# Kernel optimization log

Measured on AMD Instinct MI355X. Metric: run time of the kernel, lower is better.

## Reference

```python
import jax, jax.numpy as jnp
import numpy as np

N = 50000   # nodes
E = 600000  # edges / hyperedge incidences
D = 128     # node_in_dim
H = 128     # hidden_dim
TAU = 0.5
ALPHA = 0.5
LAM = 0.5

_PARAM_SHAPES = [('Wq0', (1, H)), ('bq0', (H,)), ('W0', (D, H)), ('b0', (H,)),
                 ('Whq0', (1, H)), ('bhq0', (H,)), ('Wh0', (D, H)), ('bh0', (H,)),
                 ('Wf0', (H, H)), ('bf0', (H,)), ('Wfh0', (H, H)), ('bfh0', (H,)),
                 ('aq0', (H,)), ('a0', (H,)), ('ahq0', (H,)), ('ah0', (H,)),
                 ('aq_', (H,)), ('a_', (H,)), ('ahq_', (H,)), ('ah_', (H,)),
                 ('Wlq', (1, H)), ('blq', (H,)), ('Wlf', (D, H)), ('blf', (H,)),
                 ('Wm1', (H, H)), ('bm1', (H,)), ('Wm2', (H, H)), ('bm2', (H,))]


def setup_inputs() -> dict:
    key = jax.random.key(0)
    ks = jax.random.split(key, 8 + len(_PARAM_SHAPES))
    inp = {}
    inp['feats'] = jax.random.normal(ks[0], (N, D), dtype=jnp.float32)
    inp['edge_index'] = jax.random.randint(ks[1], (2, E), 0, N).astype(jnp.int32)
    inp['edge_index_aug'] = jax.random.randint(ks[2], (2, E), 0, N).astype(jnp.int32)
    inp['pos'] = jax.random.randint(ks[3], (100,), 1, N).astype(jnp.int32)
    inp['q'] = 0
    for i, (nm, sh) in enumerate(_PARAM_SHAPES):
        inp[nm] = jax.random.normal(ks[4 + i], sh, dtype=jnp.float32) * 0.05
    return inp


def _forward(feats, Wq0, bq0, W0, b0, Whq0, bhq0, Wh0, bh0, Wf0, bf0, Wfh0, bfh0,
             aq0, a0, ahq0, ah0, aq_, a_, ahq_, ah_, Wlq, blq, Wlf, blf,
             Wm1, bm1, Wm2, bm2, edge_index, edge_index_aug, q, pos):
    # ---- GCNConv (PyG default: add self-loops + symmetric normalization) ----
    sl = jnp.arange(N, dtype=edge_index.dtype)
    src = jnp.concatenate([edge_index[0], sl])
    dst = jnp.concatenate([edge_index[1], sl])
    deg = jax.ops.segment_sum(jnp.ones(src.shape[0], jnp.float32), dst, num_segments=N)
    dinv = jax.lax.rsqrt(deg)  # deg >= 1 thanks to self-loops
    enorm = dinv[src] * dinv[dst]

    def gcn(x, W, b):
        xw = x @ W
        return jax.ops.segment_sum(xw[src] * enorm[:, None], dst, num_segments=N) + b

    # ---- HypergraphConv (PyG, no attention): X' = D^-1 H B^-1 H^T X W ----
    node = edge_index_aug[0]
    he = edge_index_aug[1]
    Be = jax.ops.segment_sum(jnp.ones((E,), jnp.float32), he, num_segments=N)
    Dn = jax.ops.segment_sum(jnp.ones((E,), jnp.float32), node, num_segments=N)
    Binv = jnp.where(Be > 0, 1.0 / Be, 0.0)
    Dninv = jnp.where(Dn > 0, 1.0 / Dn, 0.0)

    def hg(x, W, b):
        xw = x @ W
        me = jax.ops.segment_sum(xw[node], he, num_segments=N) * Binv[:, None]
        return jax.ops.segment_sum(me[he], node, num_segments=N) * Dninv[:, None] + b

    # ---- attention-weighted fusion of two views (softmax over 2 logits) ----
    def fuse(a, b, wa, wb):
        att = jax.nn.softmax(jnp.stack([a @ wa, b @ wb], axis=1), axis=1)  # [N,2]
        return att[:, 0:1] * a + att[:, 1:2] * b

    querys = jnp.zeros((N, 1), jnp.float32).at[q].set(1.0)
    hq = jax.nn.relu(gcn(querys, Wq0, bq0))
    h = jax.nn.relu(gcn(feats, W0, b0))
    hf = fuse(hq, h, aq0, a0)
    h_augq = jax.nn.relu(hg(querys, Whq0, bhq0))
    h_aug = jax.nn.relu(hg(feats, Wh0, bh0))
    h_augf = fuse(h_augq, h_aug, ahq0, ah0)
    querys2 = querys @ Wlq + blq
    feats2 = feats @ Wlf + blf
    hf_ = fuse(querys2, feats2, aq_, a_)
    hf = jax.nn.relu(hf + gcn(hf_, Wf0, bf0))
    hfh_ = fuse(querys2, feats2, ahq_, ah_)
    h_augf = jax.nn.relu(h_augf + hg(hfh_, Wfh0, bfh0))

    def mlp(x):
        return jax.nn.relu(x @ Wm1 + bm1) @ Wm2 + bm2

    z = mlp(hf)
    z_aug = mlp(h_augf)

    # ---- Contra loss ----
    def expcos(v, M):
        num = M @ v
        den = jnp.maximum(jnp.linalg.norm(M, axis=1) * jnp.linalg.norm(v), 1e-8)
        return jnp.exp(num / den / TAU)

    sim1 = expcos(z[q], z)
    sim_aug1 = expcos(z_aug[q], z_aug)
    sim2 = expcos(z[q], z_aug)
    sim_aug2 = expcos(z_aug[q], z)
    mask = jnp.zeros((N,), bool).at[pos].set(True).at[q].set(False)
    nmask = jnp.sum(mask).astype(jnp.float32)

    def nlm(s):  # mean over positives of -log(s_i / sum(s))
        r = jnp.log(jnp.sum(s)) - jnp.log(s)
        return jnp.sum(jnp.where(mask, r, 0.0)) / nmask

    loss_intra = 0.5 * (nlm(sim1) + nlm(sim_aug1))
    loss_inter = 0.5 * (nlm(sim2) + nlm(sim_aug2))
    z_unsup = jnp.log(jnp.sum(sim2)) - jnp.log(sim2[q])
    z_aug_unsup = jnp.log(jnp.sum(sim_aug2)) - jnp.log(sim_aug2[q])
    loss_unsup = 0.5 * z_unsup + 0.5 * z_aug_unsup
    return loss_intra + ALPHA * loss_inter + LAM * loss_unsup


def reference(feats, Wq0, bq0, W0, b0, Whq0, bhq0, Wh0, bh0, Wf0, bf0, Wfh0, bfh0,
              aq0, a0, ahq0, ah0, aq_, a_, ahq_, ah_, Wlq, blq, Wlf, blf,
              Wm1, bm1, Wm2, bm2, edge_index, edge_index_aug, q, pos):
    return _forward(feats, Wq0, bq0, W0, b0, Whq0, bhq0, Wh0, bh0, Wf0, bf0, Wfh0, bfh0,
                    aq0, a0, ahq0, ah0, aq_, a_, ahq_, ah_, Wlq, blq, Wlf, blf,
                    Wm1, bm1, Wm2, bm2, edge_index, edge_index_aug, q, pos)
```

## Files before the change

### kernel.cpp

```cpp
#include <hip/hip_runtime.h>

#define NN 50000
#define EE 600000
#define HH 128
#define TAU_INV 2.0f
#define PSZ 6250
#define CAP 48

#define BINB 512
#define BUFC 240
#define QCAP 80000
#define QPAD 16
#define WSUB 32
#define SUBN 196

typedef __attribute__((ext_vector_type(8))) short short8;
typedef __attribute__((ext_vector_type(4))) float f32x4;
typedef __attribute__((ext_vector_type(2))) float floatx2;

__device__ __forceinline__ float wsum64(float v) {
#pragma unroll
  for (int m = 32; m >= 1; m >>= 1) v += __shfl_xor(v, m, 64);
  return v;
}
__device__ __forceinline__ unsigned short f2bf(float f) {
  unsigned u = __builtin_bit_cast(unsigned, f);
  u = u + 0x7FFFu + ((u >> 16) & 1u);
  return (unsigned short)(u >> 16);
}
__device__ __forceinline__ float bf2f(unsigned short h) {
  unsigned u = ((unsigned)h) << 16;
  return __builtin_bit_cast(float, u);
}
__device__ __forceinline__ unsigned char fp8_enc1(float v) {
  int p = __builtin_amdgcn_cvt_pk_fp8_f32(v, v, 0, false);
  return (unsigned char)(p & 0xFF);
}
__device__ __forceinline__ void fp8x8_dec(uint2 v, float* f) {
  floatx2 a = __builtin_amdgcn_cvt_pk_f32_fp8(v.x, false);
  floatx2 b = __builtin_amdgcn_cvt_pk_f32_fp8(v.x, true);
  floatx2 c = __builtin_amdgcn_cvt_pk_f32_fp8(v.y, false);
  floatx2 d = __builtin_amdgcn_cvt_pk_f32_fp8(v.y, true);
  f[0] = a.x; f[1] = a.y; f[2] = b.x; f[3] = b.y;
  f[4] = c.x; f[5] = c.y; f[6] = d.x; f[7] = d.y;
}
__device__ __forceinline__ uint2 fp8x8_enc(const float* f) {
  int w0 = __builtin_amdgcn_cvt_pk_fp8_f32(f[0], f[1], 0, false);
  w0 = __builtin_amdgcn_cvt_pk_fp8_f32(f[2], f[3], w0, true);
  int w1 = __builtin_amdgcn_cvt_pk_fp8_f32(f[4], f[5], 0, false);
  w1 = __builtin_amdgcn_cvt_pk_fp8_f32(f[6], f[7], w1, true);
  return make_uint2((unsigned)w0, (unsigned)w1);
}

#define LDSW 136

__global__ __launch_bounds__(256) void bin_k(const int* __restrict__ ei,
                                             const int* __restrict__ ea,
                                             int* __restrict__ qcnt,
                                             unsigned int* __restrict__ qdata,
                                             const int* __restrict__ pos,
                                             const int* __restrict__ qp,
                                             int* __restrict__ maskI) {
  __shared__ int cnt[24], base[24], pfx[25];
  __shared__ unsigned int buf[24 * BUFC];
  const int tid = threadIdx.x;
  if (tid < 24) cnt[tid] = 0;
  if (blockIdx.x == 0 && tid < 100) maskI[pos[tid]] = 1;
  __syncthreads();
  if (blockIdx.x == 0 && tid == 0) maskI[*qp] = 0;
  for (int e = blockIdx.x * 256 + tid; e < EE; e += BINB * 256) {
    int pay0 = __builtin_nontemporal_load(ei + e);
    int k0 = __builtin_nontemporal_load(ei + EE + e);
    int pay1 = __builtin_nontemporal_load(ea + e);
    int k1 = __builtin_nontemporal_load(ea + EE + e);
    int k2 = pay1, pay2 = k1;
    int g0 = k0 / PSZ;
    int g1 = 8 + k1 / PSZ;
    int g2 = 16 + k2 / PSZ;
    int o0 = atomicAdd(&cnt[g0], 1);
    int o1 = atomicAdd(&cnt[g1], 1);
    int o2 = atomicAdd(&cnt[g2], 1);
    if (o0 < BUFC) buf[g0 * BUFC + o0] = ((unsigned)k0 << 16) | (unsigned)pay0;
    if (o1 < BUFC) buf[g1 * BUFC + o1] = ((unsigned)k1 << 16) | (unsigned)pay1;
    if (o2 < BUFC) buf[g2 * BUFC + o2] = ((unsigned)k2 << 16) | (unsigned)pay2;
  }
  __syncthreads();
  if (tid < 24) {
    int c = min(cnt[tid], BUFC);
    cnt[tid] = c;
    base[tid] = atomicAdd(&qcnt[tid * QPAD], c);
  }
  __syncthreads();
  if (tid == 0) {
    int s = 0;
#pragma unroll
    for (int g = 0; g < 24; ++g) { pfx[g] = s; s += cnt[g]; }
    pfx[24] = s;
  }
  __syncthreads();
  const int total = pfx[24];
  for (int j = tid; j < total; j += 256) {
    int lo2 = 0, hi2 = 24;
    while (lo2 + 1 < hi2) {
      int mid = (lo2 + hi2) >> 1;
      if (j >= pfx[mid]) lo2 = mid; else hi2 = mid;
    }
    int g = lo2;
    int i = j - pfx[g];
    int dq = base[g] + i;
    if (dq < QCAP) qdata[(size_t)g * QCAP + dq] = buf[g * BUFC + i];
  }
}

__global__ __launch_bounds__(256) void fillp_k(const int* __restrict__ qcnt,
                                               const unsigned int* __restrict__ qdata,
                                               int* __restrict__ cursor,
                                               unsigned short* __restrict__ slotsA,
                                               unsigned short* __restrict__ slotsB,
                                               unsigned short* __restrict__ slotsC,
                                               float* __restrict__ cntq,
                                               const int* __restrict__ qp,
                                               float* __restrict__ dinv,
                                               float* __restrict__ Binv,
                                               float* __restrict__ Dninv) {
  __shared__ int cur[SUBN];
  const int w = blockIdx.x;
  const int p = w & 7;
  const int r = (w >> 3) % 3;
  const int s = w / 24;
  const int lo = p * PSZ + s * SUBN;
  const int hi = min(lo + SUBN, (p + 1) * PSZ);
  const int tid = threadIdx.x;
  if (tid < SUBN) cur[tid] = 0;
  __syncthreads();
  const int g = r * 8 + p;
  const int qlen = min(qcnt[g * QPAD], QCAP);
  const unsigned int* qd = qdata + (size_t)g * QCAP;
  unsigned short* slots = (r == 0) ? slotsA : (r == 1) ? slotsB : slotsC;
  const int q = *qp;
  auto proc = [&](unsigned int rec) {
    int key = (int)(rec >> 16);
    if (key >= lo && key < hi) {
      int pay = (int)(rec & 0xFFFFu);
      int idx = atomicAdd(&cur[key - lo], 1);
      if (idx < CAP) slots[key * CAP + idx] = (unsigned short)pay;
      if (r == 1 && pay == q) atomicAdd(&cntq[key], 1.0f);
    }
  };
  const int nv4 = qlen >> 2;
  const uint4* qd4 = (const uint4*)qd;
  int j = tid;
  for (; j + 256 < nv4; j += 512) {
    uint4 r0 = qd4[j];
    uint4 r1 = qd4[j + 256];
    proc(r0.x); proc(r0.y); proc(r0.z); proc(r0.w);
    proc(r1.x); proc(r1.y); proc(r1.z); proc(r1.w);
  }
  if (j < nv4) {
    uint4 r0 = qd4[j];
    proc(r0.x); proc(r0.y); proc(r0.z); proc(r0.w);
  }
  int i = (nv4 << 2) + tid;
  if (i < qlen) proc(qd[i]);
  __syncthreads();
  for (int k = lo + tid; k < hi; k += 256) {
    int c = cur[k - lo];
    cursor[r * NN + k] = c;
    if (r == 0) dinv[k] = rsqrtf((float)(c + 1));
    else if (r == 1) Binv[k] = (c > 0) ? 1.0f / (float)c : 0.0f;
    else Dninv[k] = (c > 0) ? 1.0f / (float)c : 0.0f;
  }
}

__device__ __forceinline__ void shq_body(const int* __restrict__ ei, const int* __restrict__ ea,
                                         const int* __restrict__ qp,
                                         const float* __restrict__ dinv,
                                         const float* __restrict__ Binv,
                                         const float* __restrict__ cntq,
                                         float* __restrict__ s_hq, float* __restrict__ s_hgq,
                                         int bid) {
  int e = bid * 256 + threadIdx.x;
  if (e >= EE) return;
  int q = *qp;
  int src = __builtin_nontemporal_load(ei + e);
  if (src == q) {
    int dst = __builtin_nontemporal_load(ei + EE + e);
    atomicAdd(&s_hq[dst], dinv[q] * dinv[dst]);
  }
  int he = __builtin_nontemporal_load(ea + EE + e);
  float cq = cntq[he];
  if (cq != 0.0f) {
    int node = __builtin_nontemporal_load(ea + e);
    atomicAdd(&s_hgq[node], Binv[he] * cq);
  }
  if (e == 0) atomicAdd(&s_hq[q], dinv[q] * dinv[q]);
}

__device__ __forceinline__ void fuse2_body(const unsigned short* __restrict__ f2,
                                           const int* __restrict__ qp,
                                           const float* __restrict__ Wlq,
                                           const float* __restrict__ blq,
                                           const float* __restrict__ aq1,
                                           const float* __restrict__ a1,
                                           const float* __restrict__ aq2,
                                           const float* __restrict__ a2,
                                           unsigned short* __restrict__ out1,
                                           unsigned short* __restrict__ out2, int bid) {
  int row = bid * 4 + (threadIdx.x >> 6);
  if (row >= NN) return;
  int lane = threadIdx.x & 63;
  int c0 = lane, c1 = lane + 64;
  int q = *qp;
  float q20 = blq[c0] + ((row == q) ? Wlq[c0] : 0.f);
  float q21 = blq[c1] + ((row == q) ? Wlq[c1] : 0.f);
  float f0 = bf2f(f2[(size_t)row * 128 + c0]);
  float f1 = bf2f(f2[(size_t)row * 128 + c1]);
  float dq1 = wsum64(q20 * aq1[c0] + q21 * aq1[c1]);
  float df1 = wsum64(f0 * a1[c0] + f1 * a1[c1]);
  float dq2 = wsum64(q20 * aq2[c0] + q21 * aq2[c1]);
  float df2 = wsum64(f0 * a2[c0] + f1 * a2[c1]);
  {
    float mx = fmaxf(dq1, df1);
    float e0 = expf(dq1 - mx), e1 = expf(df1 - mx);
    float w0 = e0 / (e0 + e1), w1 = 1.f - w0;
    out1[(size_t)row * 128 + c0] = f2bf(w0 * q20 + w1 * f0);
    out1[(size_t)row * 128 + c1] = f2bf(w0 * q21 + w1 * f1);
  }
  {
    float mx = fmaxf(dq2, df2);
    float e0 = expf(dq2 - mx), e1 = expf(df2 - mx);
    float w0 = e0 / (e0 + e1), w1 = 1.f - w0;
    out2[(size_t)row * 128 + c0] = f2bf(w0 * q20 + w1 * f0);
    out2[(size_t)row * 128 + c1] = f2bf(w0 * q21 + w1 * f1);
  }
}

__global__ __launch_bounds__(256) void f2_k(const int* __restrict__ ei,
                                            const int* __restrict__ ea,
                                            const int* __restrict__ qp,
                                            const float* __restrict__ dinv,
                                            const float* __restrict__ Binv,
                                            const float* __restrict__ cntq,
                                            float* __restrict__ s_hq,
                                            float* __restrict__ s_hgq,
                                            const unsigned short* __restrict__ B6,
                                            const float* __restrict__ Wlq,
                                            const float* __restrict__ blq,
                                            const float* __restrict__ aq_,
                                            const float* __restrict__ a_,
                                            const float* __restrict__ ahq_,
                                            const float* __restrict__ ah_,
                                            unsigned short* __restrict__ B3,
                                            unsigned short* __restrict__ B4, int eb) {
  int b = blockIdx.x;
  if (b < eb)
    shq_body(ei, ea, qp, dinv, Binv, cntq, s_hq, s_hgq, b);
  else
    fuse2_body(B6, qp, Wlq, blq, aq_, a_, ahq_, ah_, B3, B4, b - eb);
}

__global__ void pack_k(const float* __restrict__ W0, const float* __restrict__ Wh0,
                       const float* __restrict__ Wlf, const float* __restrict__ Wf0,
                       const float* __restrict__ Wfh0, const float* __restrict__ Wm1,
                       const float* __restrict__ Wm2, unsigned short* __restrict__ out) {
  int tid = blockIdx.x * 256 + threadIdx.x;
  if (tid >= 7 * 2048) return;
  int mat = tid >> 11, r = tid & 2047;
  int s = r >> 9, c = (r >> 6) & 7, lane = r & 63;
  const float* W = (mat == 0) ? W0 : (mat == 1) ? Wh0 : (mat == 2) ? Wlf
                 : (mat == 3) ? Wf0 : (mat == 4) ? Wfh0 : (mat == 5) ? Wm1 : Wm2;
  int k0 = 32 * s + (lane >> 4) * 8;
  int n = 16 * c + (lane & 15);
  unsigned short* o = out + (size_t)tid * 8;
#pragma unroll
  for (int j = 0; j < 8; ++j) o[j] = f2bf(W[(k0 + j) * 128 + n]);
}

template <bool BIAS, bool RELU, int OM>
__device__ __forceinline__ void gemm_core(unsigned short* As, const short8* Wp,
                                          const float* bias, void* outv, int r0, int nrows,
                                          int tid) {
  const int wave = tid >> 6, lane = tid & 63;
  const int quad = lane >> 4, l15 = lane & 15;
  f32x4 acc[8];
#pragma unroll
  for (int c = 0; c < 8; ++c) acc[c] = (f32x4){0.f, 0.f, 0.f, 0.f};
#pragma unroll
  for (int s = 0; s < 4; ++s) {
    short8 a = *(const short8*)&As[(wave * 16 + l15) * LDSW + s * 32 + quad * 8];
#pragma unroll
    for (int c = 0; c < 8; ++c) {
      short8 b = Wp[(s * 8 + c) * 64 + lane];
      acc[c] = __builtin_amdgcn_mfma_f32_16x16x32_bf16(a, b, acc[c], 0, 0, 0);
    }
  }
  __syncthreads();
  const int rwl = wave * 16 + quad * 4;
  if (OM == 2) {
    unsigned char* l8 = (unsigned char*)As;
#pragma unroll
    for (int c = 0; c < 8; ++c) {
      int col = c * 16 + l15;
      float bv = BIAS ? bias[col] : 0.f;
#pragma unroll
      for (int r = 0; r < 4; ++r) {
        float v = acc[c][r] + bv;
        if (RELU) v = fmaxf(v, 0.f);
        l8[(rwl + r) * 128 + col] = fp8_enc1(v);
      }
    }
    __syncthreads();
#pragma unroll
    for (int t = 0; t < 2; ++t) {
      int idx = (t * 256 + tid) * 16;
      int row = idx >> 7, off = idx & 127;
      int grow = r0 + row;
      if (grow < nrows)
        *(uint4*)&((unsigned char*)outv)[(size_t)grow * 256 + off] = *(uint4*)&l8[idx];
    }
  } else {
    unsigned short* l16 = As;
#pragma unroll
    for (int c = 0; c < 8; ++c) {
      int col = c * 16 + l15;
      float bv = BIAS ? bias[col] : 0.f;
#pragma unroll
      for (int r = 0; r < 4; ++r) {
        float v = acc[c][r] + bv;
        if (RELU) v = fmaxf(v, 0.f);
        l16[(rwl + r) * 128 + col] = f2bf(v);
      }
    }
    __syncthreads();
#pragma unroll
    for (int t = 0; t < 4; ++t) {
      int idx = (t * 256 + tid) * 16;
      int row = idx >> 8, off = idx & 255;
      int grow = r0 + row;
      if (grow < nrows)
        *(uint4*)&((unsigned char*)outv)[(size_t)grow * 256 + off] =
            *(uint4*)&((unsigned char*)l16)[idx];
    }
  }
}

__device__ __forceinline__ void stage_bf16(const unsigned short* A, unsigned short* As,
                                           int r0, int nrows, int tid) {
#pragma unroll
  for (int t = 0; t < 4; ++t) {
    int v = t * 256 + tid;
    int row = v >> 4, cc = v & 15;
    int gr = r0 + row;
    uint4 val = make_uint4(0, 0, 0, 0);
    if (gr < nrows) val = ((const uint4*)A)[(size_t)gr * 16 + cc];
    *(uint4*)&As[row * LDSW + cc * 8] = val;
  }
}

template <bool BIAS, bool RELU, int OM>
__global__ __launch_bounds__(256) void gemm2_mfma(const unsigned short* __restrict__ A0,
                                                  const unsigned short* __restrict__ A1,
                                                  const short8* __restrict__ Wp0,
                                                  const short8* __restrict__ Wp1,
                                                  const float* __restrict__ b0,
                                                  const float* __restrict__ b1,
                                                  void* __restrict__ o0, void* __restrict__ o1,
                                                  int nrows, int nblk) {
  __shared__ unsigned short As[64 * LDSW];
  int b = blockIdx.x;
  const unsigned short* A = A0;
  const short8* Wp = Wp0;
  const float* bias = b0;
  void* o = o0;
  if (b >= nblk) {
    b -= nblk; A = A1; Wp = Wp1; bias = b1; o = o1;
  }
  const int r0 = b * 64;
  stage_bf16(A, As, r0, nrows, threadIdx.x);
  __syncthreads();
  gemm_core<BIAS, RELU, OM>(As, Wp, bias, o, r0, nrows, threadIdx.x);
}

__global__ __launch_bounds__(256) void gemm3_mfma(const float* __restrict__ A,
                                                  const short8* __restrict__ Wp,
                                                  const float* __restrict__ bias2,
                                                  unsigned char* __restrict__ p1,
                                                  unsigned char* __restrict__ p2,
                                                  unsigned short* __restrict__ out2,
                                                  int nrows) {
  __shared__ unsigned short As[64 * LDSW];
  const int tid = threadIdx.x;
  const int bh = blockIdx.x & 1;
  const int r0 = (blockIdx.x >> 1) * 64;
#pragma unroll
  for (int t = 0; t < 8; ++t) {
    int v = t * 256 + tid;
    int row = v >> 5, c4 = v & 31;
    int gr = r0 + row;
    f32x4 val = (f32x4){0.f, 0.f, 0.f, 0.f};
    if (gr < nrows) val = ((const f32x4*)A)[(size_t)gr * 32 + c4];
    ushort4 o;
    o.x = f2bf(val.x); o.y = f2bf(val.y); o.z = f2bf(val.z); o.w = f2bf(val.w);
    *(ushort4*)&As[row * LDSW + c4 * 4] = o;
  }
  __syncthreads();
  const int wave = tid >> 6, lane = tid & 63;
  const int quad = lane >> 4, l15 = lane & 15;
  f32x4 acc[3][4];
#pragma unroll
  for (int m = 0; m < 3; ++m)
#pragma unroll
    for (int c = 0; c < 4; ++c) acc[m][c] = (f32x4){0.f, 0.f, 0.f, 0.f};
#pragma unroll
  for (int s = 0; s < 4; ++s) {
    short8 a = *(const short8*)&As[(wave * 16 + l15) * LDSW + s * 32 + quad * 8];
#pragma unroll
    for (int m = 0; m < 3; ++m)
#pragma unroll
      for (int c = 0; c < 4; ++c) {
        short8 bb = Wp[(size_t)m * 2048 + (s * 8 + bh * 4 + c) * 64 + lane];
        acc[m][c] = __builtin_amdgcn_mfma_f32_16x16x32_bf16(a, bb, acc[m][c], 0, 0, 0);
      }
  }
  __syncthreads();
  unsigned char* l8a = (unsigned char*)As;
  unsigned char* l8b = l8a + 4096;
  unsigned short* l16 = (unsigned short*)(l8a + 8192);
  const int rwl = wave * 16 + quad * 4;
#pragma unroll
  for (int c = 0; c < 4; ++c) {
    int coll = c * 16 + l15;
    float bv = bias2[(bh * 4 + c) * 16 + l15];
#pragma unroll
    for (int r = 0; r < 4; ++r) {
      int lrow = rwl + r;
      l8a[lrow * 64 + coll] = fp8_enc1(acc[0][c][r]);
      l8b[lrow * 64 + coll] = fp8_enc1(acc[1][c][r]);
      l16[lrow * 64 + coll] = f2bf(acc[2][c][r] + bv);
    }
  }
  __syncthreads();
  {
    int idx = tid * 16;
    int row = idx >> 6, off = idx & 63;
    int grow = r0 + row;
    if (grow < nrows) {
      *(uint4*)&p1[(size_t)grow * 256 + bh * 64 + off] = *(uint4*)&l8a[idx];
      *(uint4*)&p2[(size_t)grow * 256 + bh * 64 + off] = *(uint4*)&l8b[idx];
    }
  }
#pragma unroll
  for (int t = 0; t < 2; ++t) {
    int idx = (t * 256 + tid) * 16;
    int row = idx >> 7, off = idx & 127;
    int grow = r0 + row;
    if (grow < nrows)
      *(uint4*)&((unsigned char*)out2)[(size_t)grow * 256 + bh * 128 + off] =
          *(uint4*)&((unsigned char*)l16)[idx];
  }
}

template <int MODE, int OUT>
__device__ __forceinline__ void gpair_body(const uint2* __restrict__ xp,
                                           uint2* __restrict__ yp,
                                           unsigned short* __restrict__ outf,
                                           const int* __restrict__ cnt,
                                           const unsigned short* __restrict__ slots,
                                           const float* __restrict__ wv,
                                           const float* __restrict__ svec,
                                           const float* __restrict__ Wq,
                                           const float* __restrict__ bq,
                                           const float* __restrict__ bm,
                                           const float* __restrict__ aq,
                                           const float* __restrict__ am,
                                           const float* __restrict__ bres, int blk) {
  int node = blk * 8 + (threadIdx.x >> 5);
  if (node >= NN) return;
  int l = threadIdx.x & 31;
  int st = node * CAP;
  int n = min(cnt[node], CAP);
  float acc[8];
#pragma unroll
  for (int i = 0; i < 8; ++i) acc[i] = 0.f;
  int p = 0;
  for (; p + 4 <= n; p += 4) {
    ushort4 s4 = *(const ushort4*)&slots[st + p];
    uint2 v0 = xp[(size_t)s4.x * 32 + l];
    uint2 v1 = xp[(size_t)s4.y * 32 + l];
    uint2 v2 = xp[(size_t)s4.z * 32 + l];
    uint2 v3 = xp[(size_t)s4.w * 32 + l];
    float f[8];
    if (MODE == 0) {
      float w0 = wv[s4.x], w1 = wv[s4.y], w2 = wv[s4.z], w3 = wv[s4.w];
      fp8x8_dec(v0, f);
#pragma unroll
      for (int i = 0; i < 8; ++i) acc[i] = fmaf(w0, f[i], acc[i]);
      fp8x8_dec(v1, f);
#pragma unroll
      for (int i = 0; i < 8; ++i) acc[i] = fmaf(w1, f[i], acc[i]);
      fp8x8_dec(v2, f);
#pragma unroll
      for (int i = 0; i < 8; ++i) acc[i] = fmaf(w2, f[i], acc[i]);
      fp8x8_dec(v3, f);
#pragma unroll
      for (int i = 0; i < 8; ++i) acc[i] = fmaf(w3, f[i], acc[i]);
    } else {
      fp8x8_dec(v0, f);
#pragma unroll
      for (int i = 0; i < 8; ++i) acc[i] += f[i];
      fp8x8_dec(v1, f);
#pragma unroll
      for (int i = 0; i < 8; ++i) acc[i] += f[i];
      fp8x8_dec(v2, f);
#pragma unroll
      for (int i = 0; i < 8; ++i) acc[i] += f[i];
      fp8x8_dec(v3, f);
#pragma unroll
      for (int i = 0; i < 8; ++i) acc[i] += f[i];
    }
  }
  for (; p < n; ++p) {
    int s = slots[st + p];
    uint2 v = xp[(size_t)s * 32 + l];
    float f[8];
    fp8x8_dec(v, f);
    if (MODE == 0) {
      float w = wv[s];
#pragma unroll
      for (int i = 0; i < 8; ++i) acc[i] = fmaf(w, f[i], acc[i]);
    } else {
#pragma unroll
      for (int i = 0; i < 8; ++i) acc[i] += f[i];
    }
  }
  float sc = wv[node];
  if (MODE == 0) {
    uint2 v = xp[(size_t)node * 32 + l];
    float f[8];
    fp8x8_dec(v, f);
#pragma unroll
    for (int i = 0; i < 8; ++i) acc[i] = sc * fmaf(sc, f[i], acc[i]);
  } else {
#pragma unroll
    for (int i = 0; i < 8; ++i) acc[i] *= sc;
  }
  if (OUT == 0) {
    yp[(size_t)node * 32 + l] = fp8x8_enc(acc);
  } else {
    float y2v[8];
#pragma unroll
    for (int i = 0; i < 8; ++i) y2v[i] = __shfl_xor(acc[i], 16, 64);
    float s = svec[node];
    if (MODE == 1) s *= sc;
    int cg = l & 15;
    float h[8], hq[8];
    float pdm = 0.f, pdq = 0.f;
#pragma unroll
    for (int i = 0; i < 8; ++i) {
      int c = cg * 8 + i;
      h[i] = fmaxf(acc[i] + bm[c], 0.f);
      hq[i] = fmaxf(fmaf(s, Wq[c], bq[c]), 0.f);
      pdm = fmaf(h[i], am[c], pdm);
      pdq = fmaf(hq[i], aq[c], pdq);
    }
#pragma unroll
    for (int m = 1; m <= 8; m <<= 1) {
      pdm += __shfl_xor(pdm, m, 64);
      pdq += __shfl_xor(pdq, m, 64);
    }
    float mx = fmaxf(pdq, pdm);
    float e0 = expf(pdq - mx), e1 = expf(pdm - mx);
    float w0 = e0 / (e0 + e1), w1 = 1.f - w0;
    if (l < 16) {
      unsigned short r[8];
#pragma unroll
      for (int i = 0; i < 8; ++i) {
        int c = cg * 8 + i;
        r[i] = f2bf(fmaxf(fmaf(w0, hq[i], fmaf(w1, h[i], y2v[i] + bres[c])), 0.f));
      }
      uint4 o;
      o.x = ((unsigned)r[1] << 16) | r[0];
      o.y = ((unsigned)r[3] << 16) | r[2];
      o.z = ((unsigned)r[5] << 16) | r[4];
      o.w = ((unsigned)r[7] << 16) | r[6];
      *(uint4*)&outf[(size_t)node * 128 + cg * 8] = o;
    }
  }
}

__global__ void dgather12_k(const uint2* __restrict__ xp1, unsigned short* __restrict__ B3,
                            const uint2* __restrict__ xp2, uint2* __restrict__ yp3,
                            const int* __restrict__ cursor,
                            const unsigned short* __restrict__ slotsA,
                            const unsigned short* __restrict__ slotsB,
                            const float* __restrict__ dinv, const float* __restrict__ Binv,
                            const float* __restrict__ s_hq, const float* __restrict__ Wq0,
                            const float* __restrict__ bq0, const float* __restrict__ b0,
                            const float* __restrict__ aq0, const float* __restrict__ a0,
                            const float* __restrict__ bf0, int nblk) {
  int b = blockIdx.x;
  if (b < nblk)
    gpair_body<0, 2>(xp1, nullptr, B3, cursor, slotsA, dinv, s_hq, Wq0, bq0, b0, aq0, a0,
                     bf0, b);
  else
    gpair_body<1, 0>(xp2, yp3, nullptr, cursor + NN, slotsB, Binv, nullptr, nullptr,
                     nullptr, nullptr, nullptr, nullptr, nullptr, b - nblk);
}

__global__ void dgather3_k(const uint2* __restrict__ xp, unsigned short* __restrict__ B4,
                           const int* __restrict__ cursor,
                           const unsigned short* __restrict__ slotsC,
                           const float* __restrict__ Dninv, const float* __restrict__ s_hgq,
                           const float* __restrict__ Whq0, const float* __restrict__ bhq0,
                           const float* __restrict__ bh0, const float* __restrict__ ahq0,
                           const float* __restrict__ ah0, const float* __restrict__ bfh0) {
  gpair_body<1, 2>(xp, nullptr, B4, cursor + 2 * NN, slotsC, Dninv, s_hgq, Whq0, bhq0, bh0,
                   ahq0, ah0, bfh0, blockIdx.x);
}

__global__ void sim_k(const unsigned short* __restrict__ z,
                      const unsigned short* __restrict__ za, const int* __restrict__ qp,
                      float4* __restrict__ simbuf, float* __restrict__ scal_out) {
  int row = blockIdx.x * 4 + (threadIdx.x >> 6);
  if (row >= NN) return;
  int lane = threadIdx.x & 63;
  int c0 = lane, c1 = lane + 64;
  int q = *qp;
  float zi0 = bf2f(z[(size_t)row * 128 + c0]), zi1 = bf2f(z[(size_t)row * 128 + c1]);
  float zai0 = bf2f(za[(size_t)row * 128 + c0]), zai1 = bf2f(za[(size_t)row * 128 + c1]);
  float zq0 = bf2f(z[(size_t)q * 128 + c0]), zq1 = bf2f(z[(size_t)q * 128 + c1]);
  float zaq0 = bf2f(za[(size_t)q * 128 + c0]), zaq1 = bf2f(za[(size_t)q * 128 + c1]);
  float nzi = wsum64(zi0 * zi0 + zi1 * zi1);
  float nzai = wsum64(zai0 * zai0 + zai1 * zai1);
  float nzq = wsum64(zq0 * zq0 + zq1 * zq1);
  float nzaq = wsum64(zaq0 * zaq0 + zaq1 * zaq1);
  float d1 = wsum64(zi0 * zq0 + zi1 * zq1);
  float d2 = wsum64(zai0 * zaq0 + zai1 * zaq1);
  float d3 = wsum64(zai0 * zq0 + zai1 * zq1);
  float d4 = wsum64(zi0 * zaq0 + zi1 * zaq1);
  if (lane == 0) {
    float ni = sqrtf(nzi), nai = sqrtf(nzai);
    float nq = sqrtf(nzq), naq = sqrtf(nzaq);
    float c1_ = d1 / fmaxf(ni * nq, 1e-8f) * TAU_INV;
    float ca1 = d2 / fmaxf(nai * naq, 1e-8f) * TAU_INV;
    float c2_ = d3 / fmaxf(nai * nq, 1e-8f) * TAU_INV;
    float ca2 = d4 / fmaxf(ni * naq, 1e-8f) * TAU_INV;
    simbuf[row] = make_float4(c1_, ca1, c2_, ca2);
    if (row == q) {
      scal_out[9] = c2_;
      scal_out[10] = ca2;
    }
  }
}

__global__ __launch_bounds__(256) void reduce_sim_k(const float4* __restrict__ simbuf,
                                                    const int* __restrict__ maskI,
                                                    float* __restrict__ scal) {
  float acc[9];
#pragma unroll
  for (int i = 0; i < 9; ++i) acc[i] = 0.f;
  for (int row = blockIdx.x * 256 + threadIdx.x; row < NN; row += gridDim.x * 256) {
    float4 v = simbuf[row];
    acc[0] += expf(v.x);
    acc[1] += expf(v.y);
    acc[2] += expf(v.z);
    acc[3] += expf(v.w);
    if (maskI[row]) {
      acc[4] += v.x; acc[5] += v.y; acc[6] += v.z; acc[7] += v.w;
      acc[8] += 1.0f;
    }
  }
  __shared__ float s[9][4];
  int lane = threadIdx.x & 63, wv = threadIdx.x >> 6;
#pragma unroll
  for (int i = 0; i < 9; ++i) {
    float r = wsum64(acc[i]);
    if (lane == 0) s[i][wv] = r;
  }
  __syncthreads();
  if (threadIdx.x < 9) {
    float r = s[threadIdx.x][0] + s[threadIdx.x][1] + s[threadIdx.x][2] + s[threadIdx.x][3];
    atomicAdd(&scal[threadIdx.x], r);
  }
}

__global__ void final_k(const float* __restrict__ scal, float* __restrict__ out) {
  if (threadIdx.x != 0 || blockIdx.x != 0) return;
  float S1 = scal[0], Sa1 = scal[1], S2 = scal[2], Sa2 = scal[3];
  float L1 = scal[4], La1 = scal[5], L2 = scal[6], La2 = scal[7];
  float NM = scal[8], Q2 = scal[9], Qa2 = scal[10];
  float intra = 0.5f * ((logf(S1) - L1 / NM) + (logf(Sa1) - La1 / NM));
  float inter = 0.5f * ((logf(S2) - L2 / NM) + (logf(Sa2) - La2 / NM));
  float unsup = 0.5f * (logf(S2) - Q2) + 0.5f * (logf(Sa2) - Qa2);
  out[0] = intra + 0.5f * inter + 0.5f * unsup;
}

extern "C" void kernel_launch(void* const* d_in, const int* in_sizes, int n_in,
                              void* d_out, int out_size, void* d_ws, size_t ws_size,
                              hipStream_t stream) {
  const float* feats = (const float*)d_in[0];
  const int* ei = (const int*)d_in[1];
  const int* ea = (const int*)d_in[2];
  const int* pos = (const int*)d_in[3];
  const int* qp = (const int*)d_in[4];
  const float* Wq0 = (const float*)d_in[5];
  const float* bq0 = (const float*)d_in[6];
  const float* W0 = (const float*)d_in[7];
  const float* b0 = (const float*)d_in[8];
  const float* Whq0 = (const float*)d_in[9];
  const float* bhq0 = (const float*)d_in[10];
  const float* Wh0 = (const float*)d_in[11];
  const float* bh0 = (const float*)d_in[12];
  const float* Wf0 = (const float*)d_in[13];
  const float* bf0 = (const float*)d_in[14];
  const float* Wfh0 = (const float*)d_in[15];
  const float* bfh0 = (const float*)d_in[16];
  const float* aq0 = (const float*)d_in[17];
  const float* a0 = (const float*)d_in[18];
  const float* ahq0 = (const float*)d_in[19];
  const float* ah0 = (const float*)d_in[20];
  const float* aq_ = (const float*)d_in[21];
  const float* a_ = (const float*)d_in[22];
  const float* ahq_ = (const float*)d_in[23];
  const float* ah_ = (const float*)d_in[24];
  const float* Wlq = (const float*)d_in[25];
  const float* blq = (const float*)d_in[26];
  const float* Wlf = (const float*)d_in[27];
  const float* blf = (const float*)d_in[28];
  const float* Wm1 = (const float*)d_in[29];
  const float* bm1 = (const float*)d_in[30];
  const float* Wm2 = (const float*)d_in[31];
  const float* bm2 = (const float*)d_in[32];

  char* ws = (char*)d_ws;
  size_t off = 0;
  auto take = [&](size_t bytes) -> void* {
    void* p = ws + off;
    off = (off + bytes + 255) & ~(size_t)255;
    return p;
  };
  int* cursor3 = (int*)take(3 * NN * 4);
  int* maskI = (int*)take(NN * 4);
  float* s_hq = (float*)take(NN * 4);
  float* cntq = (float*)take(NN * 4);
  float* s_hgq = (float*)take(NN * 4);
  float* scal = (float*)take(64 * 4);
  int* qcnt = (int*)take(24 * QPAD * 4);
  size_t zero_end = off;
  unsigned short* slotsA = (unsigned short*)take((size_t)NN * CAP * 2);
  unsigned short* slotsB = (unsigned short*)take((size_t)NN * CAP * 2);
  unsigned short* slotsC = (unsigned short*)take((size_t)NN * CAP * 2);
  unsigned int* qdata = (unsigned int*)take((size_t)24 * QCAP * 4);
  float* dinv = (float*)take(NN * 4);
  float* Binv = (float*)take(NN * 4);
  float* Dninv = (float*)take(NN * 4);
  float4* simbuf = (float4*)take((size_t)NN * 16);
  unsigned short* Wpack = (unsigned short*)take((size_t)7 * 16384 * 2);
  const size_t BFSZ = (size_t)NN * HH * 2;
  unsigned short* B0 = (unsigned short*)take(BFSZ);
  unsigned short* B1 = (unsigned short*)take(BFSZ);
  unsigned short* B2 = (unsigned short*)take(BFSZ);
  unsigned short* B3 = (unsigned short*)take(BFSZ);
  unsigned short* B4 = (unsigned short*)take(BFSZ);
  unsigned short* B5 = (unsigned short*)take(BFSZ);
  unsigned short* B6 = (unsigned short*)take(BFSZ);
  unsigned char* P1 = (unsigned char*)take((size_t)NN * 256);
  unsigned char* P2 = (unsigned char*)take((size_t)NN * 256);
  unsigned char* P3 = (unsigned char*)take((size_t)NN * 256);

  const int EB = (EE + 255) / 256;
  const int GMB = (NN + 63) / 64;
  const int GTB = (NN + 7) / 8;
  const int RB = (NN + 3) / 4;
  const short8* Wp = (const short8*)Wpack;

  hipMemsetAsync(d_ws, 0, zero_end, stream);
  pack_k<<<(7 * 2048 + 255) / 256, 256, 0, stream>>>(W0, Wh0, Wlf, Wf0, Wfh0, Wm1, Wm2,
                                                     Wpack);
  bin_k<<<BINB, 256, 0, stream>>>(ei, ea, qcnt, qdata, pos, qp, maskI);
  fillp_k<<<24 * WSUB, 256, 0, stream>>>(qcnt, qdata, cursor3, slotsA, slotsB, slotsC,
                                         cntq, qp, dinv, Binv, Dninv);
  gemm3_mfma<<<2 * GMB, 256, 0, stream>>>(feats, Wp, blf, P1, P2, B6, NN);
  f2_k<<<EB + RB, 256, 0, stream>>>(ei, ea, qp, dinv, Binv, cntq, s_hq, s_hgq, B6, Wlq,
                                    blq, aq_, a_, ahq_, ah_, B3, B4, EB);
  gemm2_mfma<false, false, 2><<<2 * GMB, 256, 0, stream>>>(
      B3, B4, Wp + (size_t)3 * 2048, Wp + (size_t)4 * 2048, nullptr, nullptr, P1 + 128,
      P2 + 128, NN, GMB);
  dgather12_k<<<2 * GTB, 256, 0, stream>>>((const uint2*)P1, B3, (const uint2*)P2,
                                           (uint2*)P3, cursor3, slotsA, slotsB, dinv, Binv,
                                           s_hq, Wq0, bq0, b0, aq0, a0, bf0, GTB);
  dgather3_k<<<GTB, 256, 0, stream>>>((const uint2*)P3, B4, cursor3, slotsC, Dninv, s_hgq,
                                      Whq0, bhq0, bh0, ahq0, ah0, bfh0);
  gemm2_mfma<true, true, 1><<<2 * GMB, 256, 0, stream>>>(
      B3, B4, Wp + (size_t)5 * 2048, Wp + (size_t)5 * 2048, bm1, bm1, B0, B1, NN, GMB);
  gemm2_mfma<true, false, 1><<<2 * GMB, 256, 0, stream>>>(
      B0, B1, Wp + (size_t)6 * 2048, Wp + (size_t)6 * 2048, bm2, bm2, B2, B5, NN, GMB);
  sim_k<<<RB, 256, 0, stream>>>(B2, B5, qp, simbuf, scal);
  reduce_sim_k<<<64, 256, 0, stream>>>(simbuf, maskI, scal);
  final_k<<<1, 64, 0, stream>>>(scal, (float*)d_out);
}
```

Before: 405.8 us.

## Fold query-scatter passes into fill and gather, fuse MLP GEMM pair

Removes the edge-parallel atomic pass that built s_hq and s_hgq. s_hq becomes a per-node count of query neighbours taken during slot filling, with the dinv factors applied in the gather. s_hgq is recomputed inside the hyperedge gather from Binv and cntq. The two back-to-back MLP GEMMs are fused into one kernel that keeps the ReLU intermediate in LDS, which drops the B0/B1 round trip through HBM and one launch. In exchange the third gather does extra scattered reads, fill_k does extra shared atomics, and the fused GEMM reads two weight sets per block.

```diff
diff --git a/kernel.cpp b/kernel.cpp
--- a/kernel.cpp
+++ b/kernel.cpp
@@ -122,8 +122,10 @@
                                                const int* __restrict__ qp,
                                                float* __restrict__ dinv,
                                                float* __restrict__ Binv,
-                                               float* __restrict__ Dninv) {
+                                               float* __restrict__ Dninv,
+                                               float* __restrict__ s_hq) {
   __shared__ int cur[SUBN];
+  __shared__ int qcur[SUBN];
   const int w = blockIdx.x;
   const int p = w & 7;
   const int r = (w >> 3) % 3;
@@ -131,7 +133,7 @@
   const int lo = p * PSZ + s * SUBN;
   const int hi = min(lo + SUBN, (p + 1) * PSZ);
   const int tid = threadIdx.x;
-  if (tid < SUBN) cur[tid] = 0;
+  if (tid < SUBN) { cur[tid] = 0; qcur[tid] = 0; }
   __syncthreads();
   const int g = r * 8 + p;
   const int qlen = min(qcnt[g * QPAD], QCAP);
@@ -144,6 +146,7 @@
       int pay = (int)(rec & 0xFFFFu);
       int idx = atomicAdd(&cur[key - lo], 1);
       if (idx < CAP) slots[key * CAP + idx] = (unsigned short)pay;
+      if (r == 0 && pay == q) atomicAdd(&qcur[key - lo], 1);
       if (r == 1 && pay == q) atomicAdd(&cntq[key], 1.0f);
     }
   };
@@ -166,47 +169,20 @@
   for (int k = lo + tid; k < hi; k += 256) {
     int c = cur[k - lo];
     cursor[r * NN + k] = c;
-    if (r == 0) dinv[k] = rsqrtf((float)(c + 1));
-    else if (r == 1) Binv[k] = (c > 0) ? 1.0f / (float)c : 0.0f;
+    if (r == 0) {
+      dinv[k] = rsqrtf((float)(c + 1));
+      s_hq[k] = (float)(qcur[k - lo] + (k == q ? 1 : 0));
+    } else if (r == 1) Binv[k] = (c > 0) ? 1.0f / (float)c : 0.0f;
     else Dninv[k] = (c > 0) ? 1.0f / (float)c : 0.0f;
   }
 }
 
-__device__ __forceinline__ void shq_body(const int* __restrict__ ei, const int* __restrict__ ea,
-                                         const int* __restrict__ qp,
-                                         const float* __restrict__ dinv,
-                                         const float* __restrict__ Binv,
-                                         const float* __restrict__ cntq,
-                                         float* __restrict__ s_hq, float* __restrict__ s_hgq,
-                                         int bid) {
-  int e = bid * 256 + threadIdx.x;
-  if (e >= EE) return;
-  int q = *qp;
-  int src = __builtin_nontemporal_load(ei + e);
-  if (src == q) {
-    int dst = __builtin_nontemporal_load(ei + EE + e);
-    atomicAdd(&s_hq[dst], dinv[q] * dinv[dst]);
-  }
-  int he = __builtin_nontemporal_load(ea + EE + e);
-  float cq = cntq[he];
-  if (cq != 0.0f) {
-    int node = __builtin_nontemporal_load(ea + e);
-    atomicAdd(&s_hgq[node], Binv[he] * cq);
-  }
-  if (e == 0) atomicAdd(&s_hq[q], dinv[q] * dinv[q]);
-}
-
-__device__ __forceinline__ void fuse2_body(const unsigned short* __restrict__ f2,
-                                           const int* __restrict__ qp,
-                                           const float* __restrict__ Wlq,
-                                           const float* __restrict__ blq,
-                                           const float* __restrict__ aq1,
-                                           const float* __restrict__ a1,
-                                           const float* __restrict__ aq2,
-                                           const float* __restrict__ a2,
-                                           unsigned short* __restrict__ out1,
-                                           unsigned short* __restrict__ out2, int bid) {
-  int row = bid * 4 + (threadIdx.x >> 6);
+__global__ void fuse2_k(const unsigned short* __restrict__ f2, const int* __restrict__ qp,
+                        const float* __restrict__ Wlq, const float* __restrict__ blq,
+                        const float* __restrict__ aq1, const float* __restrict__ a1,
+                        const float* __restrict__ aq2, const float* __restrict__ a2,
+                        unsigned short* __restrict__ out1, unsigned short* __restrict__ out2) {
+  int row = blockIdx.x * 4 + (threadIdx.x >> 6);
   if (row >= NN) return;
   int lane = threadIdx.x & 63;
   int c0 = lane, c1 = lane + 64;
@@ -235,30 +211,6 @@
   }
 }
 
-__global__ __launch_bounds__(256) void f2_k(const int* __restrict__ ei,
-                                            const int* __restrict__ ea,
-                                            const int* __restrict__ qp,
-                                            const float* __restrict__ dinv,
-                                            const float* __restrict__ Binv,
-                                            const float* __restrict__ cntq,
-                                            float* __restrict__ s_hq,
-                                            float* __restrict__ s_hgq,
-                                            const unsigned short* __restrict__ B6,
-                                            const float* __restrict__ Wlq,
-                                            const float* __restrict__ blq,
-                                            const float* __restrict__ aq_,
-                                            const float* __restrict__ a_,
-                                            const float* __restrict__ ahq_,
-                                            const float* __restrict__ ah_,
-                                            unsigned short* __restrict__ B3,
-                                            unsigned short* __restrict__ B4, int eb) {
-  int b = blockIdx.x;
-  if (b < eb)
-    shq_body(ei, ea, qp, dinv, Binv, cntq, s_hq, s_hgq, b);
-  else
-    fuse2_body(B6, qp, Wlq, blq, aq_, a_, ahq_, ah_, B3, B4, b - eb);
-}
-
 __global__ void pack_k(const float* __restrict__ W0, const float* __restrict__ Wh0,
                        const float* __restrict__ Wlf, const float* __restrict__ Wf0,
                        const float* __restrict__ Wfh0, const float* __restrict__ Wm1,
@@ -381,6 +333,78 @@
   gemm_core<BIAS, RELU, OM>(As, Wp, bias, o, r0, nrows, threadIdx.x);
 }
 
+__global__ __launch_bounds__(256) void gemm22_mfma(const unsigned short* __restrict__ A0,
+                                                   const unsigned short* __restrict__ A1,
+                                                   const short8* __restrict__ Wp1,
+                                                   const short8* __restrict__ Wp2,
+                                                   const float* __restrict__ bm1,
+                                                   const float* __restrict__ bm2,
+                                                   unsigned short* __restrict__ o0,
+                                                   unsigned short* __restrict__ o1,
+                                                   int nrows, int nblk) {
+  __shared__ unsigned short As[64 * LDSW];
+  __shared__ unsigned short Bs[64 * LDSW];
+  int b = blockIdx.x;
+  const unsigned short* A = A0;
+  unsigned short* o = o0;
+  if (b >= nblk) { b -= nblk; A = A1; o = o1; }
+  const int r0 = b * 64;
+  const int tid = threadIdx.x;
+  stage_bf16(A, As, r0, nrows, tid);
+  __syncthreads();
+  const int wave = tid >> 6, lane = tid & 63;
+  const int quad = lane >> 4, l15 = lane & 15;
+  const int rwl = wave * 16 + quad * 4;
+  f32x4 acc[8];
+#pragma unroll
+  for (int c = 0; c < 8; ++c) acc[c] = (f32x4){0.f, 0.f, 0.f, 0.f};
+#pragma unroll
+  for (int s = 0; s < 4; ++s) {
+    short8 a = *(const short8*)&As[(wave * 16 + l15) * LDSW + s * 32 + quad * 8];
+#pragma unroll
+    for (int c = 0; c < 8; ++c)
+      acc[c] = __builtin_amdgcn_mfma_f32_16x16x32_bf16(a, Wp1[(s * 8 + c) * 64 + lane],
+                                                       acc[c], 0, 0, 0);
+  }
+#pragma unroll
+  for (int c = 0; c < 8; ++c) {
+    int col = c * 16 + l15;
+    float bv = bm1[col];
+#pragma unroll
+    for (int r = 0; r < 4; ++r)
+      Bs[(rwl + r) * LDSW + col] = f2bf(fmaxf(acc[c][r] + bv, 0.f));
+  }
+  __syncthreads();
+#pragma unroll
+  for (int c = 0; c < 8; ++c) acc[c] = (f32x4){0.f, 0.f, 0.f, 0.f};
+#pragma unroll
+  for (int s = 0; s < 4; ++s) {
+    short8 a = *(const short8*)&Bs[(wave * 16 + l15) * LDSW + s * 32 + quad * 8];
+#pragma unroll
+    for (int c = 0; c < 8; ++c)
+      acc[c] = __builtin_amdgcn_mfma_f32_16x16x32_bf16(a, Wp2[(s * 8 + c) * 64 + lane],
+                                                       acc[c], 0, 0, 0);
+  }
+  unsigned short* l16 = As;
+#pragma unroll
+  for (int c = 0; c < 8; ++c) {
+    int col = c * 16 + l15;
+    float bv = bm2[col];
+#pragma unroll
+    for (int r = 0; r < 4; ++r) l16[(rwl + r) * 128 + col] = f2bf(acc[c][r] + bv);
+  }
+  __syncthreads();
+#pragma unroll
+  for (int t = 0; t < 4; ++t) {
+    int idx = (t * 256 + tid) * 16;
+    int row = idx >> 8, off = idx & 255;
+    int grow = r0 + row;
+    if (grow < nrows)
+      *(uint4*)&((unsigned char*)o)[(size_t)grow * 256 + off] =
+          *(uint4*)&((unsigned char*)l16)[idx];
+  }
+}
+
 __global__ __launch_bounds__(256) void gemm3_mfma(const float* __restrict__ A,
                                                   const short8* __restrict__ Wp,
                                                   const float* __restrict__ bias2,
@@ -460,7 +484,7 @@
   }
 }
 
-template <int MODE, int OUT>
+template <int MODE, int OUT, bool SQ>
 __device__ __forceinline__ void gpair_body(const uint2* __restrict__ xp,
                                            uint2* __restrict__ yp,
                                            unsigned short* __restrict__ outf,
@@ -468,6 +492,9 @@
                                            const unsigned short* __restrict__ slots,
                                            const float* __restrict__ wv,
                                            const float* __restrict__ svec,
+                                           const float* __restrict__ BinvT,
+                                           const float* __restrict__ cntqT,
+                                           const int* __restrict__ qp,
                                            const float* __restrict__ Wq,
                                            const float* __restrict__ bq,
                                            const float* __restrict__ bm,
@@ -482,6 +509,7 @@
   float acc[8];
 #pragma unroll
   for (int i = 0; i < 8; ++i) acc[i] = 0.f;
+  float sq = 0.f;
   int p = 0;
   for (; p + 4 <= n; p += 4) {
     ushort4 s4 = *(const ushort4*)&slots[st + p];
@@ -489,6 +517,10 @@
     uint2 v1 = xp[(size_t)s4.y * 32 + l];
     uint2 v2 = xp[(size_t)s4.z * 32 + l];
     uint2 v3 = xp[(size_t)s4.w * 32 + l];
+    if (SQ) {
+      sq += BinvT[s4.x] * cntqT[s4.x] + BinvT[s4.y] * cntqT[s4.y] +
+            BinvT[s4.z] * cntqT[s4.z] + BinvT[s4.w] * cntqT[s4.w];
+    }
     float f[8];
     if (MODE == 0) {
       float w0 = wv[s4.x], w1 = wv[s4.y], w2 = wv[s4.z], w3 = wv[s4.w];
@@ -522,6 +554,7 @@
   for (; p < n; ++p) {
     int s = slots[st + p];
     uint2 v = xp[(size_t)s * 32 + l];
+    if (SQ) sq += BinvT[s] * cntqT[s];
     float f[8];
     fp8x8_dec(v, f);
     if (MODE == 0) {
@@ -550,8 +583,9 @@
     float y2v[8];
 #pragma unroll
     for (int i = 0; i < 8; ++i) y2v[i] = __shfl_xor(acc[i], 16, 64);
-    float s = svec[node];
-    if (MODE == 1) s *= sc;
+    float s;
+    if (MODE == 0) s = svec[node] * wv[*qp] * sc;
+    else s = sq * sc;
     int cg = l & 15;
     float h[8], hq[8];
     float pdm = 0.f, pdq = 0.f;
@@ -594,28 +628,31 @@
                             const unsigned short* __restrict__ slotsA,
                             const unsigned short* __restrict__ slotsB,
                             const float* __restrict__ dinv, const float* __restrict__ Binv,
-                            const float* __restrict__ s_hq, const float* __restrict__ Wq0,
-                            const float* __restrict__ bq0, const float* __restrict__ b0,
-                            const float* __restrict__ aq0, const float* __restrict__ a0,
-                            const float* __restrict__ bf0, int nblk) {
+                            const float* __restrict__ s_hq, const int* __restrict__ qp,
+                            const float* __restrict__ Wq0, const float* __restrict__ bq0,
+                            const float* __restrict__ b0, const float* __restrict__ aq0,
+                            const float* __restrict__ a0, const float* __restrict__ bf0,
+                            int nblk) {
   int b = blockIdx.x;
   if (b < nblk)
-    gpair_body<0, 2>(xp1, nullptr, B3, cursor, slotsA, dinv, s_hq, Wq0, bq0, b0, aq0, a0,
-                     bf0, b);
+    gpair_body<0, 2, false>(xp1, nullptr, B3, cursor, slotsA, dinv, s_hq, nullptr, nullptr,
+                            qp, Wq0, bq0, b0, aq0, a0, bf0, b);
   else
-    gpair_body<1, 0>(xp2, yp3, nullptr, cursor + NN, slotsB, Binv, nullptr, nullptr,
-                     nullptr, nullptr, nullptr, nullptr, nullptr, b - nblk);
+    gpair_body<1, 0, false>(xp2, yp3, nullptr, cursor + NN, slotsB, Binv, nullptr, nullptr,
+                            nullptr, nullptr, nullptr, nullptr, nullptr, nullptr, nullptr,
+                            nullptr, b - nblk);
 }
 
 __global__ void dgather3_k(const uint2* __restrict__ xp, unsigned short* __restrict__ B4,
                            const int* __restrict__ cursor,
                            const unsigned short* __restrict__ slotsC,
-                           const float* __restrict__ Dninv, const float* __restrict__ s_hgq,
+                           const float* __restrict__ Dninv, const float* __restrict__ Binv,
+                           const float* __restrict__ cntq,
                            const float* __restrict__ Whq0, const float* __restrict__ bhq0,
                            const float* __restrict__ bh0, const float* __restrict__ ahq0,
                            const float* __restrict__ ah0, const float* __restrict__ bfh0) {
-  gpair_body<1, 2>(xp, nullptr, B4, cursor + 2 * NN, slotsC, Dninv, s_hgq, Whq0, bhq0, bh0,
-                   ahq0, ah0, bfh0, blockIdx.x);
+  gpair_body<1, 2, true>(xp, nullptr, B4, cursor + 2 * NN, slotsC, Dninv, nullptr, Binv,
+                         cntq, nullptr, Whq0, bhq0, bh0, ahq0, ah0, bfh0, blockIdx.x);
 }
 
 __global__ void sim_k(const unsigned short* __restrict__ z,
@@ -757,8 +794,6 @@
   float4* simbuf = (float4*)take((size_t)NN * 16);
   unsigned short* Wpack = (unsigned short*)take((size_t)7 * 16384 * 2);
   const size_t BFSZ = (size_t)NN * HH * 2;
-  unsigned short* B0 = (unsigned short*)take(BFSZ);
-  unsigned short* B1 = (unsigned short*)take(BFSZ);
   unsigned short* B2 = (unsigned short*)take(BFSZ);
   unsigned short* B3 = (unsigned short*)take(BFSZ);
   unsigned short* B4 = (unsigned short*)take(BFSZ);
@@ -768,7 +803,6 @@
   unsigned char* P2 = (unsigned char*)take((size_t)NN * 256);
   unsigned char* P3 = (unsigned char*)take((size_t)NN * 256);
 
-  const int EB = (EE + 255) / 256;
   const int GMB = (NN + 63) / 64;
   const int GTB = (NN + 7) / 8;
   const int RB = (NN + 3) / 4;
@@ -779,22 +813,20 @@
                                                      Wpack);
   bin_k<<<BINB, 256, 0, stream>>>(ei, ea, qcnt, qdata, pos, qp, maskI);
   fillp_k<<<24 * WSUB, 256, 0, stream>>>(qcnt, qdata, cursor3, slotsA, slotsB, slotsC,
-                                         cntq, qp, dinv, Binv, Dninv);
+                                         cntq, qp, dinv, Binv, Dninv, s_hq);
   gemm3_mfma<<<2 * GMB, 256, 0, stream>>>(feats, Wp, blf, P1, P2, B6, NN);
-  f2_k<<<EB + RB, 256, 0, stream>>>(ei, ea, qp, dinv, Binv, cntq, s_hq, s_hgq, B6, Wlq,
-                                    blq, aq_, a_, ahq_, ah_, B3, B4, EB);
+  fuse2_k<<<RB, 256, 0, stream>>>(B6, qp, Wlq, blq, aq_, a_, ahq_, ah_, B3, B4);
   gemm2_mfma<false, false, 2><<<2 * GMB, 256, 0, stream>>>(
       B3, B4, Wp + (size_t)3 * 2048, Wp + (size_t)4 * 2048, nullptr, nullptr, P1 + 128,
       P2 + 128, NN, GMB);
   dgather12_k<<<2 * GTB, 256, 0, stream>>>((const uint2*)P1, B3, (const uint2*)P2,
                                            (uint2*)P3, cursor3, slotsA, slotsB, dinv, Binv,
-                                           s_hq, Wq0, bq0, b0, aq0, a0, bf0, GTB);
-  dgather3_k<<<GTB, 256, 0, stream>>>((const uint2*)P3, B4, cursor3, slotsC, Dninv, s_hgq,
-                                      Whq0, bhq0, bh0, ahq0, ah0, bfh0);
-  gemm2_mfma<true, true, 1><<<2 * GMB, 256, 0, stream>>>(
-      B3, B4, Wp + (size_t)5 * 2048, Wp + (size_t)5 * 2048, bm1, bm1, B0, B1, NN, GMB);
-  gemm2_mfma<true, false, 1><<<2 * GMB, 256, 0, stream>>>(
-      B0, B1, Wp + (size_t)6 * 2048, Wp + (size_t)6 * 2048, bm2, bm2, B2, B5, NN, GMB);
+                                           s_hq, qp, Wq0, bq0, b0, aq0, a0, bf0, GTB);
+  dgather3_k<<<GTB, 256, 0, stream>>>((const uint2*)P3, B4, cursor3, slotsC, Dninv, Binv,
+                                      cntq, Whq0, bhq0, bh0, ahq0, ah0, bfh0);
+  gemm22_mfma<<<2 * GMB, 256, 0, stream>>>(B3, B4, Wp + (size_t)5 * 2048,
+                                           Wp + (size_t)6 * 2048, bm1, bm2, B2, B5, NN,
+                                           GMB);
   sim_k<<<RB, 256, 0, stream>>>(B2, B5, qp, simbuf, scal);
   reduce_sim_k<<<64, 256, 0, stream>>>(simbuf, maskI, scal);
   final_k<<<1, 64, 0, stream>>>(scal, (float*)d_out);
```

Result: no change. 401.2 us (median of 2 runs) (-1.1%).
